# Kernel optimization log

Measured on AMD Instinct MI355X. Metric: run time of the kernel, lower is better.

Reference implementation:

```python
import jax, jax.numpy as jnp
import numpy as np

OBS_LEN, PRED_LEN = 20, 30
H, EMB, MLP, NOISE, HEADS = 32, 16, 64, 8, 4
N, B, G = 131072, 4096, 32  # total agents, scenes, agents per scene
NEG = -1e9


def layernorm(x, g, b, eps=1e-5):
    m = x.mean(-1, keepdims=True)
    v = ((x - m) ** 2).mean(-1, keepdims=True)
    return (x - m) / jnp.sqrt(v + eps) * g + b


def setup_inputs():
    key = jax.random.key(0)
    ks = iter(jax.random.split(key, 40))
    rn = lambda shape, s=0.1: jax.random.normal(next(ks), shape, jnp.float32) * s
    starts = np.arange(B, dtype=np.int64) * G
    return {
        "obs_traj": rn((OBS_LEN, N, 2), 1.0),
        "obs_traj_rel": rn((OBS_LEN, N, 2), 1.0),
        "start_end_seq": jnp.stack([jnp.asarray(starts), jnp.asarray(starts + G)], 1).astype(jnp.int32),
        "noise_z": rn((NOISE,), 1.0),
        "enc_emb_w": rn((EMB, 2)), "enc_emb_b": rn((EMB,)),
        "enc_wih": rn((4 * H, EMB)), "enc_whh": rn((4 * H, H)),
        "enc_bih": rn((4 * H,)), "enc_bhh": rn((4 * H,)),
        "lne_g": jnp.ones((H,), jnp.float32), "lne_b": jnp.zeros((H,), jnp.float32),
        "wq": rn((H, H)), "wk": rn((H, H)), "wv": rn((H, H)), "wo": rn((H, H)),
        "lnc_g": jnp.ones((2 * H,), jnp.float32), "lnc_b": jnp.zeros((2 * H,), jnp.float32),
        "mlp1_w": rn((MLP, 2 * H)), "mlp1_b": rn((MLP,)),
        "mlp2_w": rn((H - NOISE, MLP)), "mlp2_b": rn((H - NOISE,)),
        "dec_emb_w": rn((EMB, 2)), "dec_emb_b": rn((EMB,)),
        "dec_wih": rn((4 * H, EMB)), "dec_whh": rn((4 * H, H)),
        "dec_bih": rn((4 * H,)), "dec_bhh": rn((4 * H,)),
        "dec_out_w": rn((2, H)), "dec_out_b": rn((2,)),
    }


def _forward(obs_traj, obs_traj_rel, noise_z,
             enc_emb_w, enc_emb_b, enc_wih, enc_whh, enc_bih, enc_bhh,
             lne_g, lne_b, wq, wk, wv, wo, lnc_g, lnc_b,
             mlp1_w, mlp1_b, mlp2_w, mlp2_b,
             dec_emb_w, dec_emb_b, dec_wih, dec_whh, dec_bih, dec_bhh,
             dec_out_w, dec_out_b, se_np):
    n = obs_traj_rel.shape[1]
    # ---- Encoder: linear spatial embedding + single-layer LSTM over obs window
    emb = obs_traj_rel @ enc_emb_w.T + enc_emb_b  # (T, n, EMB)

    def enc_step(carry, x):
        h, c = carry
        gates = x @ enc_wih.T + enc_bih + h @ enc_whh.T + enc_bhh
        i, f, g, o = jnp.split(gates, 4, -1)
        c = jax.nn.sigmoid(f) * c + jax.nn.sigmoid(i) * jnp.tanh(g)
        h = jax.nn.sigmoid(o) * jnp.tanh(c)
        return (h, c), None

    z0 = jnp.zeros((n, H), emb.dtype)
    (h_enc, _), _ = jax.lax.scan(enc_step, (z0, z0), emb)
    h_enc = layernorm(h_enc, lne_g, lne_b)  # (n, H)

    # ---- Ragged per-scene self-attention, padded to max scene size
    lengths = se_np[:, 1] - se_np[:, 0]
    L = int(lengths.max())
    pos = np.arange(L)
    mask = pos[None, :] < lengths[:, None]                # (B, L) valid slots
    idx = np.where(mask, se_np[:, :1] + pos[None, :], 0)  # (B, L)
    Hp = h_enc[jnp.asarray(idx)]                          # (B, L, H)
    b = mask.shape[0]
    dh = H // HEADS

    def heads(w):
        return (Hp @ w.T).reshape(b, L, HEADS, dh).transpose(0, 2, 1, 3)

    q, k, v = heads(wq), heads(wk), heads(wv)
    scores = jnp.einsum('bhqd,bhkd->bhqk', q, k) / jnp.sqrt(jnp.float32(dh))
    scores = jnp.where(jnp.asarray(mask)[:, None, None, :], scores, NEG)
    attn = jnp.einsum('bhqk,bhkd->bhqd', jax.nn.softmax(scores, -1), v)
    attn = attn.transpose(0, 2, 1, 3).reshape(b, L, H) @ wo.T  # (B, L, H)
    flat = jnp.asarray(np.where(mask, idx, n).reshape(-1))     # invalid -> pad row n
    attn_s = jnp.zeros((n + 1, H), attn.dtype).at[flat].set(attn.reshape(-1, H))[:n]

    # ---- Decoder context MLP (LeakyReLU after every Linear, incl. last) + noise
    ctx = layernorm(jnp.concatenate([h_enc, attn_s], -1), lnc_g, lnc_b)
    x = jax.nn.leaky_relu(ctx @ mlp1_w.T + mlp1_b)
    x = jax.nn.leaky_relu(x @ mlp2_w.T + mlp2_b)  # (n, H-NOISE)
    dec_h = jnp.concatenate([x, jnp.broadcast_to(noise_z, (n, NOISE))], -1)
    dec_c = jnp.zeros_like(dec_h)

    # ---- Temporal decoder: LSTM rollout of PRED_LEN relative displacements
    def dec_step(carry, _):
        h, c, last_rel = carry
        e = last_rel @ dec_emb_w.T + dec_emb_b
        gates = e @ dec_wih.T + dec_bih + h @ dec_whh.T + dec_bhh
        i, f, g, o = jnp.split(gates, 4, -1)
        c = jax.nn.sigmoid(f) * c + jax.nn.sigmoid(i) * jnp.tanh(g)
        h = jax.nn.sigmoid(o) * jnp.tanh(c)
        rel = h @ dec_out_w.T + dec_out_b
        return (h, c, rel), rel

    _, preds = jax.lax.scan(dec_step, (dec_h, dec_c, obs_traj_rel[-1]), None, length=PRED_LEN)
    return preds  # (PRED_LEN, n, 2)


def reference(obs_traj, obs_traj_rel, start_end_seq, noise_z,
              enc_emb_w, enc_emb_b, enc_wih, enc_whh, enc_bih, enc_bhh,
              lne_g, lne_b, wq, wk, wv, wo, lnc_g, lnc_b,
              mlp1_w, mlp1_b, mlp2_w, mlp2_b,
              dec_emb_w, dec_emb_b, dec_wih, dec_whh, dec_bih, dec_bhh,
              dec_out_w, dec_out_b):
    se_np = np.asarray(start_end_seq)
    return _forward(obs_traj, obs_traj_rel, noise_z,
                    enc_emb_w, enc_emb_b, enc_wih, enc_whh, enc_bih, enc_bhh,
                    lne_g, lne_b, wq, wk, wv, wo, lnc_g, lnc_b,
                    mlp1_w, mlp1_b, mlp2_w, mlp2_b,
                    dec_emb_w, dec_emb_b, dec_wih, dec_whh, dec_bih, dec_bhh,
                    dec_out_w, dec_out_b, se_np)
```

## Files before the change

### kernel.cpp

```cpp
#include <hip/hip_runtime.h>
#include <hip/hip_bf16.h>
#include <stdint.h>

typedef unsigned short u16;
typedef unsigned int   u32;

#define NTOT 131072

typedef __bf16 bf16x8 __attribute__((ext_vector_type(8)));
typedef float  f32x4  __attribute__((ext_vector_type(4)));

typedef bf16x8 bf16x8_a __attribute__((may_alias));
typedef int4   int4_a   __attribute__((may_alias));
typedef u16    u16_a    __attribute__((may_alias));
typedef u32    u32_a    __attribute__((may_alias));
typedef float  f32_a    __attribute__((may_alias));
typedef float4 float4_a __attribute__((may_alias));
typedef float2 float2_a __attribute__((may_alias));
typedef f32x4  f32x4_a  __attribute__((may_alias));

__device__ __forceinline__ void lds_fence(){
  asm volatile("s_waitcnt lgkmcnt(0)" ::: "memory");
}

__device__ __forceinline__ float b2f(u16 u){ return __uint_as_float(((u32)u)<<16); }
__device__ __forceinline__ u16 f2b(float f){
  u32 x = __float_as_uint(f);
  return (u16)((x + 0x7fffu + ((x>>16)&1u)) >> 16);
}
__device__ __forceinline__ u16 bfb(float f){
  union { __bf16 b; u16 u; } c; c.b = (__bf16)f; return c.u;
}
__device__ __forceinline__ u32 pkbf(float a, float b){
  u32 r; asm("v_cvt_pk_bf16_f32 %0, %1, %2" : "=v"(r) : "v"(a), "v"(b)); return r;
}
__device__ __forceinline__ u32 pk2(float a, float b){ return pkbf(a, b); }
__device__ __forceinline__ void pack_hilo2(float a, float b, u32& whi, u32& wlo){
  whi = pkbf(a, b);
  float l0 = a - __uint_as_float(whi << 16);
  float l1 = b - __uint_as_float(whi & 0xffff0000u);
  wlo = pkbf(l0, l1);
}
__device__ __forceinline__ float ex2(float x){
  float r; asm("v_exp_f32 %0, %1" : "=v"(r) : "v"(x)); return r;
}
__device__ __forceinline__ float ld(const u16* p, long long i, bool f32m){
  return f32m ? ((const f32_a*)p)[i] : b2f(((const u16_a*)p)[i]);
}
__device__ __forceinline__ float2 ld2(const u16* p, long long i, bool f32m){
  if (f32m) return ((const float2_a*)(const void*)p)[i];
  u32 v = ((const u32_a*)p)[i];
  float2 r; r.x = b2f((u16)(v & 0xffffu)); r.y = b2f((u16)(v >> 16)); return r;
}
__device__ __forceinline__ bool is_f32(const u16* ones){
  return ((const u32_a*)ones)[0] == 0x3F800000u;
}

__device__ __forceinline__ void lstm_cell2(float i2, float f2, float g2, float o2,
                                           float& cs, float& h){
  const float K = 2.8853900817779268f;
  float ai = ex2(i2);
  float ef = ex2(f2);
  float gc = fminf(fmaxf(g2, -80.f), 80.f);
  float tg = ex2(gc);
  float t1  = (1.f+ai)*(tg+1.f);
  float efp = 1.f+ef;
  float num = cs*t1 + K*((tg-1.f)*efp);
  cs = num * __builtin_amdgcn_rcpf(efp*t1);
  float ao = ex2(o2);
  float tc = ex2(cs);
  h = (tc-1.f) * __builtin_amdgcn_rcpf((1.f+ao)*(tc+1.f));
}

__device__ __forceinline__ bf16x8 mk_frag(const u16* W, int ldW, int n, int kbase, bool f32m){
  union { bf16x8 v; u16 s[8]; } u;
  if (f32m){
    const f32_a* p = (const f32_a*)W + (size_t)n*ldW + kbase;
    float4 x0 = *reinterpret_cast<const float4_a*>(p);
    float4 x1 = *reinterpret_cast<const float4_a*>(p+4);
    u.s[0]=f2b(x0.x); u.s[1]=f2b(x0.y); u.s[2]=f2b(x0.z); u.s[3]=f2b(x0.w);
    u.s[4]=f2b(x1.x); u.s[5]=f2b(x1.y); u.s[6]=f2b(x1.z); u.s[7]=f2b(x1.w);
  } else {
    #pragma unroll
    for (int j=0;j<8;++j) u.s[j] = ((const u16_a*)W)[(size_t)n*ldW + kbase + j];
  }
  return u.v;
}
__device__ __forceinline__ void split_hilo(const float* x, bf16x8& hi, bf16x8& lo){
  union { bf16x8 v; u16 s[8]; } uh, ul;
  #pragma unroll
  for (int j=0;j<8;++j){ u16 hb=f2b(x[j]); uh.s[j]=hb; ul.s[j]=f2b(x[j]-b2f(hb)); }
  hi=uh.v; lo=ul.v;
}

__global__ void prep_kernel(const u16* __restrict__ wih, const u16* __restrict__ whh,
                            const u16* __restrict__ bih, const u16* __restrict__ bhh,
                            const u16* __restrict__ dwih, const u16* __restrict__ dwhh,
                            const u16* __restrict__ dbih, const u16* __restrict__ dbhh,
                            const u16* __restrict__ dembw, const u16* __restrict__ dembb,
                            const u16* __restrict__ doutw, const u16* __restrict__ doutb,
                            const u16* __restrict__ lng,
                            u16* __restrict__ WTe, u16* __restrict__ WTd,
                            float* __restrict__ biasd, float* __restrict__ wemo)
{
  const bool f32m = is_f32(lng);
  const float Lc = 1.4426950408889634f;
  int tid = blockIdx.x*blockDim.x + threadIdx.x;
  int nthr = gridDim.x*blockDim.x;
  for (int idx = tid; idx < 128*96; idx += nthr){
    int rw = idx/96, k = idx - rw*96;
    const float sc = ((rw >> 5) == 2) ? 2.f*Lc : -Lc;
    float ve;
    if (k < 64){
      int kc = k & 31; int q = kc >> 3, r = kc & 7;
      int u = (r < 4) ? (q*4 + r) : (16 + q*4 + (r-4));
      ve = sc*ld(whh, rw*32+u, f32m);
    } else {
      int kk = k - 64; int q = kk >> 3, j = kk & 7;
      if (j < 4){
        ve = sc*ld(wih, rw*16 + q*4+j, f32m);
      } else if (q == 0 && j == 4){
        ve = sc*(ld(bih, rw, f32m) + ld(bhh, rw, f32m));
      } else if (q == 0 && j == 5){
        float bse = sc*(ld(bih, rw, f32m) + ld(bhh, rw, f32m));
        ve = bse - b2f(f2b(bse));
      } else {
        ve = 0.f;
      }
    }
    WTe[idx] = f2b(ve);
    if (k < 64){
      int kc = k & 31; int q = kc >> 3, r = kc & 7;
      int u = (r < 4) ? (q*4 + r) : (16 + q*4 + (r-4));
      float wem0 = 0.f, wem1 = 0.f;
      #pragma unroll
      for (int j=0; j<16; ++j){
        float wv = ld(dwih, rw*16+j, f32m);
        wem0 += wv*ld(dembw, j*2,   f32m);
        wem1 += wv*ld(dembw, j*2+1, f32m);
      }
      float wp = sc*(ld(dwhh, rw*32+u, f32m)
               + wem0*ld(doutw, u,    f32m)
               + wem1*ld(doutw, 32+u, f32m));
      u16 hi = f2b(wp);
      WTd[rw*64 + k] = (k < 32) ? hi : f2b(wp - b2f(hi));
    }
  }
  if (tid < 128){
    int rw = tid;
    const float sc = ((rw >> 5) == 2) ? 2.f*Lc : -Lc;
    float wem0 = 0.f, wem1 = 0.f, wdb = 0.f;
    #pragma unroll
    for (int j=0; j<16; ++j){
      float wv = ld(dwih, rw*16+j, f32m);
      wem0 += wv*ld(dembw, j*2,   f32m);
      wem1 += wv*ld(dembw, j*2+1, f32m);
      wdb  += wv*ld(dembb, j,     f32m);
    }
    float bp = ld(dbih, rw, f32m) + ld(dbhh, rw, f32m) + wdb
             + wem0*ld(doutb, 0, f32m) + wem1*ld(doutb, 1, f32m);
    biasd[rw] = sc*bp;
    wemo[rw*2]   = sc*wem0;
    wemo[rw*2+1] = sc*wem1;
  }
}

__global__ __launch_bounds__(256, 1) void enc_kernel(
    const u16* __restrict__ obs_rel, const u16* __restrict__ WT,
    const u16* __restrict__ embw, const u16* __restrict__ embb,
    const u16* __restrict__ lng, const u16* __restrict__ lnb,
    float* __restrict__ hln)
{
  const bool f32m = is_f32(lng);
  const int lane = threadIdx.x & 63;
  const int wvi  = threadIdx.x >> 6;
  const int col  = lane & 15;
  const int quad = lane >> 4;
  const int base = (blockIdx.x*4 + wvi)*16;

  bf16x8 wf[8][3];
  #pragma unroll
  for (int g=0; g<8; ++g)
    #pragma unroll
    for (int c=0; c<3; ++c)
      wf[g][c] = *reinterpret_cast<const bf16x8_a*>(WT + (g*16+col)*96 + c*32 + quad*8);

  float ew0[4], ew1[4], ebv[4];
  #pragma unroll
  for (int jj=0; jj<4; ++jj){
    int j = quad*4+jj;
    ew0[jj]=ld(embw, j*2, f32m); ew1[jj]=ld(embw, j*2+1, f32m); ebv[jj]=ld(embb, j, f32m);
  }
  const u32 onespk = (quad == 0) ? 0x3F803F80u : 0u;

  union FR { bf16x8 v; u32 w[4]; };
  FR x0, x1, x2;
  x0.w[0]=x0.w[1]=x0.w[2]=x0.w[3]=0;
  x1.w[0]=x1.w[1]=x1.w[2]=x1.w[3]=0;
  x2.w[2] = onespk; x2.w[3] = 0;

  float c0[4]={0,0,0,0}, c1[4]={0,0,0,0};
  float hA[4]={0,0,0,0}, hB[4]={0,0,0,0};

  float2 rv = ld2(obs_rel, (long long)(base + col), f32m);

  #pragma unroll 1
  for (int t=0; t<20; ++t){
    float2 rnx = rv;
    if (t < 19) rnx = ld2(obs_rel, (long long)(t+1)*NTOT + base + col, f32m);
    float e0 = ew0[0]*rv.x + ew1[0]*rv.y + ebv[0];
    float e1 = ew0[1]*rv.x + ew1[1]*rv.y + ebv[1];
    float e2 = ew0[2]*rv.x + ew1[2]*rv.y + ebv[2];
    float e3 = ew0[3]*rv.x + ew1[3]*rv.y + ebv[3];
    x2.w[0] = pkbf(e0, e1);
    x2.w[1] = pkbf(e2, e3);

    f32x4 acc[8];
    #pragma unroll
    for (int g=0; g<8; ++g){ f32x4 zz = {0.f,0.f,0.f,0.f};
      acc[g] = __builtin_amdgcn_mfma_f32_16x16x32_bf16(wf[g][0], x0.v, zz, 0,0,0); }
    #pragma unroll
    for (int g=0; g<8; ++g)
      acc[g] = __builtin_amdgcn_mfma_f32_16x16x32_bf16(wf[g][1], x1.v, acc[g], 0,0,0);
    #pragma unroll
    for (int g=0; g<8; ++g)
      acc[g] = __builtin_amdgcn_mfma_f32_16x16x32_bf16(wf[g][2], x2.v, acc[g], 0,0,0);

    #pragma unroll
    for (int reg=0; reg<4; ++reg){
      lstm_cell2(acc[0][reg], acc[2][reg], acc[4][reg], acc[6][reg], c0[reg], hA[reg]);
      lstm_cell2(acc[1][reg], acc[3][reg], acc[5][reg], acc[7][reg], c1[reg], hB[reg]);
    }
    pack_hilo2(hA[0], hA[1], x0.w[0], x1.w[0]);
    pack_hilo2(hA[2], hA[3], x0.w[1], x1.w[1]);
    pack_hilo2(hB[0], hB[1], x0.w[2], x1.w[2]);
    pack_hilo2(hB[2], hB[3], x0.w[3], x1.w[3]);
    rv = rnx;
  }

  float sm = 0.f, sq = 0.f;
  #pragma unroll
  for (int reg=0; reg<4; ++reg){
    sm += hA[reg]+hB[reg];
    sq += hA[reg]*hA[reg]+hB[reg]*hB[reg];
  }
  sm += __shfl_xor(sm, 16, 64); sm += __shfl_xor(sm, 32, 64);
  sq += __shfl_xor(sq, 16, 64); sq += __shfl_xor(sq, 32, 64);
  float mean = sm*(1.f/32.f);
  float var  = sq*(1.f/32.f) - mean*mean;
  float rstd = rsqrtf(fmaxf(var, 0.f) + 1e-5f);
  float4 yA, yB;
  {
    float gA0=ld(lng,quad*4+0,f32m), gA1=ld(lng,quad*4+1,f32m), gA2=ld(lng,quad*4+2,f32m), gA3=ld(lng,quad*4+3,f32m);
    float bA0=ld(lnb,quad*4+0,f32m), bA1=ld(lnb,quad*4+1,f32m), bA2=ld(lnb,quad*4+2,f32m), bA3=ld(lnb,quad*4+3,f32m);
    float gB0=ld(lng,16+quad*4+0,f32m), gB1=ld(lng,16+quad*4+1,f32m), gB2=ld(lng,16+quad*4+2,f32m), gB3=ld(lng,16+quad*4+3,f32m);
    float bB0=ld(lnb,16+quad*4+0,f32m), bB1=ld(lnb,16+quad*4+1,f32m), bB2=ld(lnb,16+quad*4+2,f32m), bB3=ld(lnb,16+quad*4+3,f32m);
    yA.x=(hA[0]-mean)*rstd*gA0+bA0; yA.y=(hA[1]-mean)*rstd*gA1+bA1;
    yA.z=(hA[2]-mean)*rstd*gA2+bA2; yA.w=(hA[3]-mean)*rstd*gA3+bA3;
    yB.x=(hB[0]-mean)*rstd*gB0+bB0; yB.y=(hB[1]-mean)*rstd*gB1+bB1;
    yB.z=(hB[2]-mean)*rstd*gB2+bB2; yB.w=(hB[3]-mean)*rstd*gB3+bB3;
  }
  size_t a = (size_t)(base + col);
  *reinterpret_cast<float4_a*>(hln + a*32 + quad*4)      = yA;
  *reinterpret_cast<float4_a*>(hln + a*32 + 16 + quad*4) = yB;
}

__global__ __launch_bounds__(256, 1) void mid_kernel(
    const int* __restrict__ se, const float* __restrict__ hln,
    const u16* __restrict__ wq, const u16* __restrict__ wk,
    const u16* __restrict__ wvp, const u16* __restrict__ wo,
    const u16* __restrict__ lncg, const u16* __restrict__ lncb,
    const u16* __restrict__ m1w, const u16* __restrict__ m1b,
    const u16* __restrict__ m2w, const u16* __restrict__ m2b,
    const u16* __restrict__ noise, float* __restrict__ dech0)
{
  __shared__ float hsL[2][32][36];
  __shared__ float kL [2][32][36];
  __shared__ float vL [2][32][36];
  __shared__ float qL [2][32][36];
  __shared__ float aoL[2][32][36];
  __shared__ float cxL[4][16][68];

  const bool f32m = is_f32(lncg);
  const int lane = threadIdx.x & 63;
  const int wvi  = threadIdx.x >> 6;
  const int col  = lane & 15;
  const int quad = lane >> 4;
  const int sc_l = wvi >> 1;
  const int half = wvi & 1;
  const int a_lo = half*16;
  const int scene = blockIdx.x*2 + sc_l;

  const int s0  = se[2*scene];
  int len = se[2*scene+1] - s0;
  if (len > 32) len = 32; if (len < 0) len = 0;

  {
    int ar = a_lo + (lane>>2);
    long long g = (long long)s0 + ar;
    if (g > NTOT-1) g = NTOT-1; if (g < 0) g = 0;
    const f32_a* src = (const f32_a*)hln + g*32 + (lane&3)*8;
    float4 x0 = *reinterpret_cast<const float4_a*>(src);
    float4 x1 = *reinterpret_cast<const float4_a*>(src+4);
    float* dst = &hsL[sc_l][ar][(lane&3)*8];
    *reinterpret_cast<float4_a*>(dst)   = x0;
    *reinterpret_cast<float4_a*>(dst+4) = x1;
  }
  lds_fence();
  f32x4 z = {0.f,0.f,0.f,0.f};
  f32x4 qa0,qa1,ka0,ka1,va0,va1;
  {
    float hv[8];
    const float* r = &hsL[sc_l][a_lo+col][quad*8];
    float4 x0 = *reinterpret_cast<const float4_a*>(r);
    float4 x1 = *reinterpret_cast<const float4_a*>(r+4);
    hv[0]=x0.x; hv[1]=x0.y; hv[2]=x0.z; hv[3]=x0.w;
    hv[4]=x1.x; hv[5]=x1.y; hv[6]=x1.z; hv[7]=x1.w;
    bf16x8 ah, al; split_hilo(hv, ah, al);
    bf16x8 wqf0 = mk_frag(wq, 32, col,    quad*8, f32m);
    bf16x8 wqf1 = mk_frag(wq, 32, 16+col, quad*8, f32m);
    bf16x8 wkf0 = mk_frag(wk, 32, col,    quad*8, f32m);
    bf16x8 wkf1 = mk_frag(wk, 32, 16+col, quad*8, f32m);
    bf16x8 wvf0 = mk_frag(wvp,32, col,    quad*8, f32m);
    bf16x8 wvf1 = mk_frag(wvp,32, 16+col, quad*8, f32m);
    qa0 = __builtin_amdgcn_mfma_f32_16x16x32_bf16(ah, wqf0, z, 0,0,0);
    qa0 = __builtin_amdgcn_mfma_f32_16x16x32_bf16(al, wqf0, qa0, 0,0,0);
    qa1 = __builtin_amdgcn_mfma_f32_16x16x32_bf16(ah, wqf1, z, 0,0,0);
    qa1 = __builtin_amdgcn_mfma_f32_16x16x32_bf16(al, wqf1, qa1, 0,0,0);
    ka0 = __builtin_amdgcn_mfma_f32_16x16x32_bf16(ah, wkf0, z, 0,0,0);
    ka0 = __builtin_amdgcn_mfma_f32_16x16x32_bf16(al, wkf0, ka0, 0,0,0);
    ka1 = __builtin_amdgcn_mfma_f32_16x16x32_bf16(ah, wkf1, z, 0,0,0);
    ka1 = __builtin_amdgcn_mfma_f32_16x16x32_bf16(al, wkf1, ka1, 0,0,0);
    va0 = __builtin_amdgcn_mfma_f32_16x16x32_bf16(ah, wvf0, z, 0,0,0);
    va0 = __builtin_amdgcn_mfma_f32_16x16x32_bf16(al, wvf0, va0, 0,0,0);
    va1 = __builtin_amdgcn_mfma_f32_16x16x32_bf16(ah, wvf1, z, 0,0,0);
    va1 = __builtin_amdgcn_mfma_f32_16x16x32_bf16(al, wvf1, va1, 0,0,0);
  }
  #pragma unroll
  for (int reg=0; reg<4; ++reg){
    int ar = a_lo + quad*4 + reg;
    qL[sc_l][ar][col]    = qa0[reg];  qL[sc_l][ar][col+16] = qa1[reg];
    kL[sc_l][ar][col]    = ka0[reg];  kL[sc_l][ar][col+16] = ka1[reg];
    vL[sc_l][ar][col]    = va0[reg];  vL[sc_l][ar][col+16] = va1[reg];
  }
  __syncthreads();

  {
    int rid = half*64 + lane;
    int h  = rid >> 5, qa = rid & 31;
    const float* qrow = &qL[sc_l][qa][h*8];
    float4 q0 = *reinterpret_cast<const float4_a*>(qrow);
    float4 q1 = *reinterpret_cast<const float4_a*>(qrow+4);
    float p[32]; float mx = -3.4e38f;
    const float scale = 0.35355339059327373f;
    #pragma unroll
    for (int ka2=0; ka2<32; ++ka2){
      const float* kr = &kL[sc_l][ka2][h*8];
      float4 k0 = *reinterpret_cast<const float4_a*>(kr);
      float4 k1 = *reinterpret_cast<const float4_a*>(kr+4);
      float s = q0.x*k0.x + q0.y*k0.y + q0.z*k0.z + q0.w*k0.w
              + q1.x*k1.x + q1.y*k1.y + q1.z*k1.z + q1.w*k1.w;
      s *= scale;
      if (ka2 >= len) s = -1e9f;
      p[ka2] = s; mx = fmaxf(mx, s);
    }
    float ssum = 0.f;
    #pragma unroll
    for (int ka2=0; ka2<32; ++ka2){ float e = __expf(p[ka2]-mx); p[ka2]=e; ssum+=e; }
    float inv = __builtin_amdgcn_rcpf(ssum);
    float4 o0 = {0,0,0,0}, o1 = {0,0,0,0};
    #pragma unroll
    for (int ka2=0; ka2<32; ++ka2){
      const float* vr = &vL[sc_l][ka2][h*8];
      float4 v0 = *reinterpret_cast<const float4_a*>(vr);
      float4 v1 = *reinterpret_cast<const float4_a*>(vr+4);
      float w = p[ka2]*inv;
      o0.x += w*v0.x; o0.y += w*v0.y; o0.z += w*v0.z; o0.w += w*v0.w;
      o1.x += w*v1.x; o1.y += w*v1.y; o1.z += w*v1.z; o1.w += w*v1.w;
    }
    float* ar_ = &aoL[sc_l][qa][h*8];
    *reinterpret_cast<float4_a*>(ar_)   = o0;
    *reinterpret_cast<float4_a*>(ar_+4) = o1;
  }
  __syncthreads();

  f32x4 at0, at1;
  {
    float av[8];
    const float* r = &aoL[sc_l][a_lo+col][quad*8];
    float4 x0 = *reinterpret_cast<const float4_a*>(r);
    float4 x1 = *reinterpret_cast<const float4_a*>(r+4);
    av[0]=x0.x; av[1]=x0.y; av[2]=x0.z; av[3]=x0.w;
    av[4]=x1.x; av[5]=x1.y; av[6]=x1.z; av[7]=x1.w;
    bf16x8 aoh, aol; split_hilo(av, aoh, aol);
    bf16x8 wof0 = mk_frag(wo, 32, col,    quad*8, f32m);
    bf16x8 wof1 = mk_frag(wo, 32, 16+col, quad*8, f32m);
    at0 = __builtin_amdgcn_mfma_f32_16x16x32_bf16(aoh, wof0, z, 0,0,0);
    at0 = __builtin_amdgcn_mfma_f32_16x16x32_bf16(aol, wof0, at0, 0,0,0);
    at1 = __builtin_amdgcn_mfma_f32_16x16x32_bf16(aoh, wof1, z, 0,0,0);
    at1 = __builtin_amdgcn_mfma_f32_16x16x32_bf16(aol, wof1, at1, 0,0,0);
  }
  {
    float h0[4], h1[4], sm[4], sq[4];
    #pragma unroll
    for (int reg=0; reg<4; ++reg){
      int ar = a_lo + quad*4 + reg;
      h0[reg] = hsL[sc_l][ar][col];
      h1[reg] = hsL[sc_l][ar][col+16];
      float a0v = at0[reg], a1v = at1[reg];
      sm[reg] = h0[reg]+h1[reg]+a0v+a1v;
      sq[reg] = h0[reg]*h0[reg]+h1[reg]*h1[reg]+a0v*a0v+a1v*a1v;
    }
    #pragma unroll
    for (int m=1; m<16; m<<=1){
      #pragma unroll
      for (int reg=0; reg<4; ++reg){
        sm[reg] += __shfl_xor(sm[reg], m, 64);
        sq[reg] += __shfl_xor(sq[reg], m, 64);
      }
    }
    float g0=ld(lncg,col,f32m),    g1=ld(lncg,col+16,f32m);
    float g2=ld(lncg,col+32,f32m), g3=ld(lncg,col+48,f32m);
    float b0=ld(lncb,col,f32m),    b1=ld(lncb,col+16,f32m);
    float b2=ld(lncb,col+32,f32m), b3=ld(lncb,col+48,f32m);
    #pragma unroll
    for (int reg=0; reg<4; ++reg){
      float mean = sm[reg]*(1.f/64.f);
      float var  = sq[reg]*(1.f/64.f) - mean*mean;
      float rstd = rsqrtf(fmaxf(var,0.f) + 1e-5f);
      float* cr = &cxL[wvi][quad*4+reg][0];
      cr[col]    = (h0[reg] -mean)*rstd*g0 + b0;
      cr[col+16] = (h1[reg] -mean)*rstd*g1 + b1;
      cr[col+32] = (at0[reg]-mean)*rstd*g2 + b2;
      cr[col+48] = (at1[reg]-mean)*rstd*g3 + b3;
    }
  }
  lds_fence();
  f32x4 x1a[4];
  {
    float cv0[8], cv1[8];
    const float* r = &cxL[wvi][col][quad*8];
    float4 a0v = *reinterpret_cast<const float4_a*>(r);
    float4 a1v = *reinterpret_cast<const float4_a*>(r+4);
    const float* r2 = &cxL[wvi][col][32+quad*8];
    float4 b0v = *reinterpret_cast<const float4_a*>(r2);
    float4 b1v = *reinterpret_cast<const float4_a*>(r2+4);
    cv0[0]=a0v.x; cv0[1]=a0v.y; cv0[2]=a0v.z; cv0[3]=a0v.w;
    cv0[4]=a1v.x; cv0[5]=a1v.y; cv0[6]=a1v.z; cv0[7]=a1v.w;
    cv1[0]=b0v.x; cv1[1]=b0v.y; cv1[2]=b0v.z; cv1[3]=b0v.w;
    cv1[4]=b1v.x; cv1[5]=b1v.y; cv1[6]=b1v.z; cv1[7]=b1v.w;
    bf16x8 c0h,c0l,c1h,c1l;
    split_hilo(cv0, c0h, c0l);
    split_hilo(cv1, c1h, c1l);
    #pragma unroll
    for (int t=0; t<4; ++t){
      bf16x8 bfr0 = mk_frag(m1w, 64, t*16+col, quad*8,    f32m);
      bf16x8 bfr1 = mk_frag(m1w, 64, t*16+col, 32+quad*8, f32m);
      f32x4 acc = __builtin_amdgcn_mfma_f32_16x16x32_bf16(c0h, bfr0, z, 0,0,0);
      acc = __builtin_amdgcn_mfma_f32_16x16x32_bf16(c1h, bfr1, acc, 0,0,0);
      acc = __builtin_amdgcn_mfma_f32_16x16x32_bf16(c0l, bfr0, acc, 0,0,0);
      acc = __builtin_amdgcn_mfma_f32_16x16x32_bf16(c1l, bfr1, acc, 0,0,0);
      x1a[t] = acc;
    }
  }
  lds_fence();
  {
    #pragma unroll
    for (int t=0; t<4; ++t){
      float bv = ld(m1b, t*16+col, f32m);
      #pragma unroll
      for (int reg=0; reg<4; ++reg){
        float v = x1a[t][reg] + bv;
        v = (v > 0.f) ? v : 0.01f*v;
        cxL[wvi][quad*4+reg][t*16+col] = v;
      }
    }
  }
  lds_fence();
  {
    float yv0[8], yv1[8];
    const float* r = &cxL[wvi][col][quad*8];
    float4 a0v = *reinterpret_cast<const float4_a*>(r);
    float4 a1v = *reinterpret_cast<const float4_a*>(r+4);
    const float* r2 = &cxL[wvi][col][32+quad*8];
    float4 b0v = *reinterpret_cast<const float4_a*>(r2);
    float4 b1v = *reinterpret_cast<const float4_a*>(r2+4);
    yv0[0]=a0v.x; yv0[1]=a0v.y; yv0[2]=a0v.z; yv0[3]=a0v.w;
    yv0[4]=a1v.x; yv0[5]=a1v.y; yv0[6]=a1v.z; yv0[7]=a1v.w;
    yv1[0]=b0v.x; yv1[1]=b0v.y; yv1[2]=b0v.z; yv1[3]=b0v.w;
    yv1[4]=b1v.x; yv1[5]=b1v.y; yv1[6]=b1v.z; yv1[7]=b1v.w;
    bf16x8 y0h,y0l,y1h,y1l;
    split_hilo(yv0, y0h, y0l);
    split_hilo(yv1, y1h, y1l);
    f32x4 x2a[2];
    #pragma unroll
    for (int t=0; t<2; ++t){
      int n = t*16 + col; if (n > 23) n = 23;
      bf16x8 bfr0 = mk_frag(m2w, 64, n, quad*8,    f32m);
      bf16x8 bfr1 = mk_frag(m2w, 64, n, 32+quad*8, f32m);
      f32x4 acc = __builtin_amdgcn_mfma_f32_16x16x32_bf16(y0h, bfr0, z, 0,0,0);
      acc = __builtin_amdgcn_mfma_f32_16x16x32_bf16(y1h, bfr1, acc, 0,0,0);
      acc = __builtin_amdgcn_mfma_f32_16x16x32_bf16(y0l, bfr0, acc, 0,0,0);
      acc = __builtin_amdgcn_mfma_f32_16x16x32_bf16(y1l, bfr1, acc, 0,0,0);
      x2a[t] = acc;
    }
    float mb0 = ld(m2b, col, f32m);
    float mb1 = (col < 8) ? ld(m2b, 16+col, f32m) : 0.f;
    float nz  = (col >= 8) ? ld(noise, col-8, f32m) : 0.f;
    #pragma unroll
    for (int reg=0; reg<4; ++reg){
      int a32 = a_lo + quad*4 + reg;
      if (a32 < len){
        size_t g = ((size_t)(s0 + a32))*32;
        float v0 = x2a[0][reg] + mb0;
        v0 = (v0 > 0.f) ? v0 : 0.01f*v0;
        float v1;
        if (col < 8){
          v1 = x2a[1][reg] + mb1;
          v1 = (v1 > 0.f) ? v1 : 0.01f*v1;
        } else {
          v1 = nz;
        }
        dech0[g + col]      = v0;
        dech0[g + 16 + col] = v1;
      }
    }
  }
}

__global__ __launch_bounds__(256, 1) void dec_kernel(
    const u16* __restrict__ obs_rel, const u16* __restrict__ WT,
    const float* __restrict__ biasd, const float* __restrict__ wem,
    const u16* __restrict__ doutw, const u16* __restrict__ doutb,
    const float* __restrict__ h0in, const u16* __restrict__ lng,
    u16* __restrict__ out)
{
  const bool f32m = is_f32(lng);
  const int lane = threadIdx.x & 63;
  const int wvi  = threadIdx.x >> 6;
  const int col  = lane & 15;
  const int quad = lane >> 4;
  const int base = (blockIdx.x*4 + wvi)*16;

  bf16x8 wfA[8], wfB[8];
  #pragma unroll
  for (int g=0; g<8; ++g){
    wfA[g] = *reinterpret_cast<const bf16x8_a*>(WT + (g*16+col)*64 + quad*8);
    wfB[g] = *reinterpret_cast<const bf16x8_a*>(WT + (g*16+col)*64 + 32 + quad*8);
  }
  bf16x8 wouth, woutl;
  {
    union { bf16x8 v; u16 s[8]; } wh_, wl_;
    #pragma unroll
    for (int j=0; j<8; ++j){
      int u = (j < 4) ? (quad*4 + j) : (16 + quad*4 + (j-4));
      float w = (col < 2) ? ld(doutw, col*32 + u, f32m) : 0.f;
      u16 hb = f2b(w);
      wh_.s[j] = hb; wl_.s[j] = f2b(w - b2f(hb));
    }
    wouth = wh_.v; woutl = wl_.v;
  }
  f32x4 pc = {0.f,0.f,0.f,0.f};
  if (quad == 0){ pc[0] = ld(doutb,0,f32m); pc[1] = ld(doutb,1,f32m); }

  union FR { bf16x8 v; u32 w[4]; };
  FR x0, x1;
  {
    const f32_a* hp = (const f32_a*)h0in + (size_t)(base+col)*32;
    f32x4 hA4 = *(const f32x4_a*)(hp + quad*4);
    f32x4 hB4 = *(const f32x4_a*)(hp + 16 + quad*4);
    pack_hilo2(hA4[0], hA4[1], x0.w[0], x1.w[0]);
    pack_hilo2(hA4[2], hA4[3], x0.w[1], x1.w[1]);
    pack_hilo2(hB4[0], hB4[1], x0.w[2], x1.w[2]);
    pack_hilo2(hB4[2], hB4[3], x0.w[3], x1.w[3]);
  }
  float2 rv = ld2(obs_rel, (long long)19*NTOT + base + col, f32m);

  f32x4 biasr[8];
  #pragma unroll
  for (int g=0; g<8; ++g)
    biasr[g] = *(const f32x4_a*)(biasd + g*16 + quad*4);

  f32x4 cf[8];
  {
    f32x4 a2 = __builtin_amdgcn_mfma_f32_16x16x32_bf16(wouth, x0.v, pc, 0,0,0);
    a2 = __builtin_amdgcn_mfma_f32_16x16x32_bf16(wouth, x1.v, a2, 0,0,0);
    a2 = __builtin_amdgcn_mfma_f32_16x16x32_bf16(woutl, x0.v, a2, 0,0,0);
    float p0b = __shfl(a2[0], col, 64);
    float p1b = __shfl(a2[1], col, 64);
    float d0 = rv.x - p0b;
    float d1 = rv.y - p1b;
    #pragma unroll
    for (int g=0; g<8; ++g){
      const float4_a* wp = (const float4_a*)(wem + (size_t)(g*16 + quad*4)*2);
      float4 wa = wp[0], wb = wp[1];
      cf[g][0] = biasr[g][0] + wa.x*d0 + wa.y*d1;
      cf[g][1] = biasr[g][1] + wa.z*d0 + wa.w*d1;
      cf[g][2] = biasr[g][2] + wb.x*d0 + wb.y*d1;
      cf[g][3] = biasr[g][3] + wb.z*d0 + wb.w*d1;
    }
  }

  float c0[4]={0,0,0,0}, c1[4]={0,0,0,0};
  float hA[4], hB[4];

  auto dstep = [&](const f32x4 (&cin)[8], int t){
    f32x4 acc[8];
    #pragma unroll
    for (int g=0; g<8; ++g)
      acc[g] = __builtin_amdgcn_mfma_f32_16x16x32_bf16(wfA[g], x0.v, cin[g], 0,0,0);
    #pragma unroll
    for (int g=0; g<8; ++g)
      acc[g] = __builtin_amdgcn_mfma_f32_16x16x32_bf16(wfA[g], x1.v, acc[g], 0,0,0);
    #pragma unroll
    for (int g=0; g<8; ++g)
      acc[g] = __builtin_amdgcn_mfma_f32_16x16x32_bf16(wfB[g], x0.v, acc[g], 0,0,0);

    #pragma unroll
    for (int reg=0; reg<4; ++reg){
      lstm_cell2(acc[0][reg], acc[2][reg], acc[4][reg], acc[6][reg], c0[reg], hA[reg]);
      lstm_cell2(acc[1][reg], acc[3][reg], acc[5][reg], acc[7][reg], c1[reg], hB[reg]);
    }
    pack_hilo2(hA[0], hA[1], x0.w[0], x1.w[0]);
    pack_hilo2(hA[2], hA[3], x0.w[1], x1.w[1]);
    pack_hilo2(hB[0], hB[1], x0.w[2], x1.w[2]);
    pack_hilo2(hB[2], hB[3], x0.w[3], x1.w[3]);

    f32x4 a2 = __builtin_amdgcn_mfma_f32_16x16x32_bf16(wouth, x0.v, pc, 0,0,0);
    a2 = __builtin_amdgcn_mfma_f32_16x16x32_bf16(wouth, x1.v, a2, 0,0,0);
    a2 = __builtin_amdgcn_mfma_f32_16x16x32_bf16(woutl, x0.v, a2, 0,0,0);

    if (quad == 0){
      size_t idx = (size_t)(t*NTOT + base + col);
      if (f32m){
        float2 v; v.x = a2[0]; v.y = a2[1];
        *reinterpret_cast<float2_a*>((f32_a*)out + idx*2) = v;
      } else {
        *reinterpret_cast<u32_a*>(out + idx*2) = pkbf(a2[0], a2[1]);
      }
    }
  };

  dstep(cf, 0);
  #pragma unroll 1
  for (int t=1; t<30; ++t) dstep(biasr, t);
}

extern "C" void kernel_launch(void* const* d_in, const int* in_sizes, int n_in,
                              void* d_out, int out_size, void* d_ws, size_t ws_size,
                              hipStream_t stream)
{
  (void)in_sizes; (void)n_in; (void)out_size; (void)ws_size;
  const u16* obs_rel = (const u16*)d_in[1];
  const int* se      = (const int*)d_in[2];
  const u16* noise   = (const u16*)d_in[3];
  const u16* eembw = (const u16*)d_in[4];
  const u16* eembb = (const u16*)d_in[5];
  const u16* ewih  = (const u16*)d_in[6];
  const u16* ewhh  = (const u16*)d_in[7];
  const u16* ebih  = (const u16*)d_in[8];
  const u16* ebhh  = (const u16*)d_in[9];
  const u16* lneg  = (const u16*)d_in[10];
  const u16* lneb  = (const u16*)d_in[11];
  const u16* wq    = (const u16*)d_in[12];
  const u16* wk    = (const u16*)d_in[13];
  const u16* wvw   = (const u16*)d_in[14];
  const u16* wo    = (const u16*)d_in[15];
  const u16* lncg  = (const u16*)d_in[16];
  const u16* lncb  = (const u16*)d_in[17];
  const u16* m1w   = (const u16*)d_in[18];
  const u16* m1b   = (const u16*)d_in[19];
  const u16* m2w   = (const u16*)d_in[20];
  const u16* m2b   = (const u16*)d_in[21];
  const u16* dembw = (const u16*)d_in[22];
  const u16* dembb = (const u16*)d_in[23];
  const u16* dwih  = (const u16*)d_in[24];
  const u16* dwhh  = (const u16*)d_in[25];
  const u16* dbih  = (const u16*)d_in[26];
  const u16* dbhh  = (const u16*)d_in[27];
  const u16* doutw = (const u16*)d_in[28];
  const u16* doutb = (const u16*)d_in[29];

  char* ws = (char*)d_ws;
  u16*   WTe   = (u16*)(ws + 0);
  u16*   WTd   = (u16*)(ws + 24576);
  float* biasd = (float*)(ws + 40960);
  float* wem   = (float*)(ws + 41472);
  float* hln   = (float*)(ws + 65536);
  float* dech0 = (float*)(ws + 65536 + (size_t)NTOT*32*4);

  prep_kernel<<<48, 256, 0, stream>>>(ewih, ewhh, ebih, ebhh, dwih, dwhh, dbih, dbhh,
                                      dembw, dembb, doutw, doutb, lneg,
                                      WTe, WTd, biasd, wem);
  enc_kernel<<<NTOT/64, 256, 0, stream>>>(obs_rel, WTe, eembw, eembb, lneg, lneb, hln);
  mid_kernel<<<2048, 256, 0, stream>>>(se, hln, wq, wk, wvw, wo, lncg, lncb,
                                       m1w, m1b, m2w, m2b, noise, dech0);
  dec_kernel<<<NTOT/64, 256, 0, stream>>>(obs_rel, WTd, biasd, wem, doutw, doutb,
                                          dech0, lneg, (u16*)d_out);
}
```

Baseline: 478.3 us.

## Interleave two independent agent tiles per wave in decoder LSTM to hide latency

Each decoder wave now handles 32 agents as two 16-agent tiles (P and Q) and software-pipelines them. One tile's gate MFMAs are issued while the other tile's LSTM cell nonlinearities and output projection run. The grid is halved to match. This is meant to hide the serial MFMA-to-VALU dependency latency of the recurrence, at the cost of more registers per thread and fewer waves in flight.

New measurement: 502.1 us. 1.05x slower.

```diff
diff --git a/kernel.cpp b/kernel.cpp
--- a/kernel.cpp
+++ b/kernel.cpp
@@ -540,7 +540,7 @@
   const int wvi  = threadIdx.x >> 6;
   const int col  = lane & 15;
   const int quad = lane >> 4;
-  const int base = (blockIdx.x*4 + wvi)*16;
+  const int base = (blockIdx.x*4 + wvi)*32;
 
   bf16x8 wfA[8], wfB[8];
   #pragma unroll
@@ -564,48 +564,63 @@
   if (quad == 0){ pc[0] = ld(doutb,0,f32m); pc[1] = ld(doutb,1,f32m); }
 
   union FR { bf16x8 v; u32 w[4]; };
-  FR x0, x1;
-  {
-    const f32_a* hp = (const f32_a*)h0in + (size_t)(base+col)*32;
-    f32x4 hA4 = *(const f32x4_a*)(hp + quad*4);
-    f32x4 hB4 = *(const f32x4_a*)(hp + 16 + quad*4);
-    pack_hilo2(hA4[0], hA4[1], x0.w[0], x1.w[0]);
-    pack_hilo2(hA4[2], hA4[3], x0.w[1], x1.w[1]);
-    pack_hilo2(hB4[0], hB4[1], x0.w[2], x1.w[2]);
-    pack_hilo2(hB4[2], hB4[3], x0.w[3], x1.w[3]);
-  }
-  float2 rv = ld2(obs_rel, (long long)19*NTOT + base + col, f32m);
+  FR xP0, xP1, xQ0, xQ1;
+  {
+    const f32_a* hpP = (const f32_a*)h0in + (size_t)(base+col)*32;
+    f32x4 a4 = *(const f32x4_a*)(hpP + quad*4);
+    f32x4 b4 = *(const f32x4_a*)(hpP + 16 + quad*4);
+    pack_hilo2(a4[0], a4[1], xP0.w[0], xP1.w[0]);
+    pack_hilo2(a4[2], a4[3], xP0.w[1], xP1.w[1]);
+    pack_hilo2(b4[0], b4[1], xP0.w[2], xP1.w[2]);
+    pack_hilo2(b4[2], b4[3], xP0.w[3], xP1.w[3]);
+    const f32_a* hpQ = (const f32_a*)h0in + (size_t)(base+16+col)*32;
+    f32x4 c4 = *(const f32x4_a*)(hpQ + quad*4);
+    f32x4 d4 = *(const f32x4_a*)(hpQ + 16 + quad*4);
+    pack_hilo2(c4[0], c4[1], xQ0.w[0], xQ1.w[0]);
+    pack_hilo2(c4[2], c4[3], xQ0.w[1], xQ1.w[1]);
+    pack_hilo2(d4[0], d4[1], xQ0.w[2], xQ1.w[2]);
+    pack_hilo2(d4[2], d4[3], xQ0.w[3], xQ1.w[3]);
+  }
+  float2 rvP = ld2(obs_rel, (long long)19*NTOT + base + col,      f32m);
+  float2 rvQ = ld2(obs_rel, (long long)19*NTOT + base + 16 + col, f32m);
 
   f32x4 biasr[8];
   #pragma unroll
   for (int g=0; g<8; ++g)
     biasr[g] = *(const f32x4_a*)(biasd + g*16 + quad*4);
 
-  f32x4 cf[8];
-  {
-    f32x4 a2 = __builtin_amdgcn_mfma_f32_16x16x32_bf16(wouth, x0.v, pc, 0,0,0);
-    a2 = __builtin_amdgcn_mfma_f32_16x16x32_bf16(wouth, x1.v, a2, 0,0,0);
-    a2 = __builtin_amdgcn_mfma_f32_16x16x32_bf16(woutl, x0.v, a2, 0,0,0);
-    float p0b = __shfl(a2[0], col, 64);
-    float p1b = __shfl(a2[1], col, 64);
-    float d0 = rv.x - p0b;
-    float d1 = rv.y - p1b;
+  f32x4 cfP[8], cfQ[8];
+  {
+    f32x4 aP = __builtin_amdgcn_mfma_f32_16x16x32_bf16(wouth, xP0.v, pc, 0,0,0);
+    aP = __builtin_amdgcn_mfma_f32_16x16x32_bf16(wouth, xP1.v, aP, 0,0,0);
+    aP = __builtin_amdgcn_mfma_f32_16x16x32_bf16(woutl, xP0.v, aP, 0,0,0);
+    f32x4 aQ = __builtin_amdgcn_mfma_f32_16x16x32_bf16(wouth, xQ0.v, pc, 0,0,0);
+    aQ = __builtin_amdgcn_mfma_f32_16x16x32_bf16(wouth, xQ1.v, aQ, 0,0,0);
+    aQ = __builtin_amdgcn_mfma_f32_16x16x32_bf16(woutl, xQ0.v, aQ, 0,0,0);
+    float p0P = __shfl(aP[0], col, 64), p1P = __shfl(aP[1], col, 64);
+    float p0Q = __shfl(aQ[0], col, 64), p1Q = __shfl(aQ[1], col, 64);
+    float d0P = rvP.x - p0P, d1P = rvP.y - p1P;
+    float d0Q = rvQ.x - p0Q, d1Q = rvQ.y - p1Q;
     #pragma unroll
     for (int g=0; g<8; ++g){
       const float4_a* wp = (const float4_a*)(wem + (size_t)(g*16 + quad*4)*2);
       float4 wa = wp[0], wb = wp[1];
-      cf[g][0] = biasr[g][0] + wa.x*d0 + wa.y*d1;
-      cf[g][1] = biasr[g][1] + wa.z*d0 + wa.w*d1;
-      cf[g][2] = biasr[g][2] + wb.x*d0 + wb.y*d1;
-      cf[g][3] = biasr[g][3] + wb.z*d0 + wb.w*d1;
-    }
-  }
-
-  float c0[4]={0,0,0,0}, c1[4]={0,0,0,0};
-  float hA[4], hB[4];
-
-  auto dstep = [&](const f32x4 (&cin)[8], int t){
-    f32x4 acc[8];
+      cfP[g][0] = biasr[g][0] + wa.x*d0P + wa.y*d1P;
+      cfP[g][1] = biasr[g][1] + wa.z*d0P + wa.w*d1P;
+      cfP[g][2] = biasr[g][2] + wb.x*d0P + wb.y*d1P;
+      cfP[g][3] = biasr[g][3] + wb.z*d0P + wb.w*d1P;
+      cfQ[g][0] = biasr[g][0] + wa.x*d0Q + wa.y*d1Q;
+      cfQ[g][1] = biasr[g][1] + wa.z*d0Q + wa.w*d1Q;
+      cfQ[g][2] = biasr[g][2] + wb.x*d0Q + wb.y*d1Q;
+      cfQ[g][3] = biasr[g][3] + wb.z*d0Q + wb.w*d1Q;
+    }
+  }
+
+  float cP0[4]={0,0,0,0}, cP1[4]={0,0,0,0};
+  float cQ0[4]={0,0,0,0}, cQ1[4]={0,0,0,0};
+  f32x4 accP[8], accQ[8];
+
+  auto gates = [&](const FR& x0, const FR& x1, const f32x4* cin, f32x4* acc){
     #pragma unroll
     for (int g=0; g<8; ++g)
       acc[g] = __builtin_amdgcn_mfma_f32_16x16x32_bf16(wfA[g], x0.v, cin[g], 0,0,0);
@@ -615,7 +630,10 @@
     #pragma unroll
     for (int g=0; g<8; ++g)
       acc[g] = __builtin_amdgcn_mfma_f32_16x16x32_bf16(wfB[g], x0.v, acc[g], 0,0,0);
-
+  };
+  auto cps = [&](const f32x4* acc, float* c0, float* c1, FR& x0, FR& x1,
+                 int t, int cofs){
+    float hA[4], hB[4];
     #pragma unroll
     for (int reg=0; reg<4; ++reg){
       lstm_cell2(acc[0][reg], acc[2][reg], acc[4][reg], acc[6][reg], c0[reg], hA[reg]);
@@ -625,13 +643,11 @@
     pack_hilo2(hA[2], hA[3], x0.w[1], x1.w[1]);
     pack_hilo2(hB[0], hB[1], x0.w[2], x1.w[2]);
     pack_hilo2(hB[2], hB[3], x0.w[3], x1.w[3]);
-
     f32x4 a2 = __builtin_amdgcn_mfma_f32_16x16x32_bf16(wouth, x0.v, pc, 0,0,0);
     a2 = __builtin_amdgcn_mfma_f32_16x16x32_bf16(wouth, x1.v, a2, 0,0,0);
     a2 = __builtin_amdgcn_mfma_f32_16x16x32_bf16(woutl, x0.v, a2, 0,0,0);
-
     if (quad == 0){
-      size_t idx = (size_t)(t*NTOT + base + col);
+      size_t idx = (size_t)(t*NTOT + base + cofs + col);
       if (f32m){
         float2 v; v.x = a2[0]; v.y = a2[1];
         *reinterpret_cast<float2_a*>((f32_a*)out + idx*2) = v;
@@ -641,9 +657,21 @@
     }
   };
 
-  dstep(cf, 0);
+  gates(xP0, xP1, cfP, accP);
+  gates(xQ0, xQ1, cfQ, accQ);
+  cps(accP, cP0, cP1, xP0, xP1, 0, 0);
+  gates(xP0, xP1, biasr, accP);
+  cps(accQ, cQ0, cQ1, xQ0, xQ1, 0, 16);
   #pragma unroll 1
-  for (int t=1; t<30; ++t) dstep(biasr, t);
+  for (int t=1; t<29; ++t){
+    gates(xQ0, xQ1, biasr, accQ);
+    cps(accP, cP0, cP1, xP0, xP1, t, 0);
+    gates(xP0, xP1, biasr, accP);
+    cps(accQ, cQ0, cQ1, xQ0, xQ1, t, 16);
+  }
+  gates(xQ0, xQ1, biasr, accQ);
+  cps(accP, cP0, cP1, xP0, xP1, 29, 0);
+  cps(accQ, cQ0, cQ1, xQ0, xQ1, 29, 16);
 }
 
 extern "C" void kernel_launch(void* const* d_in, const int* in_sizes, int n_in,
@@ -695,6 +723,6 @@
   enc_kernel<<<NTOT/64, 256, 0, stream>>>(obs_rel, WTe, eembw, eembb, lneg, lneb, hln);
   mid_kernel<<<2048, 256, 0, stream>>>(se, hln, wq, wk, wvw, wo, lncg, lncb,
                                        m1w, m1b, m2w, m2b, noise, dech0);
-  dec_kernel<<<NTOT/64, 256, 0, stream>>>(obs_rel, WTd, biasd, wem, doutw, doutb,
-                                          dech0, lneg, (u16*)d_out);
-}
+  dec_kernel<<<NTOT/128, 256, 0, stream>>>(obs_rel, WTd, biasd, wem, doutw, doutb,
+                                           dech0, lneg, (u16*)d_out);
+}
```
